# Optimization experiments

Hardware: AMD Instinct MI355X
Metric: run time of the kernel (lower is better)

The kernel has to match this reference:

```python
import jax, jax.numpy as jnp
import numpy as np
from jax import lax

B, L, H, O, T = 256, 2, 256, 256, 512


def setup_inputs() -> dict:
    key = jax.random.key(0)
    ks = jax.random.split(key, 9)
    s = 0.1  # keep gates out of saturation
    return {
        "x": jax.random.normal(ks[0], (B, 1, H), jnp.float32),
        "h0": jax.random.normal(ks[1], (L, B, H), jnp.float32) * s,
        "c0": jax.random.normal(ks[2], (L, B, H), jnp.float32) * s,
        "W_ih": jax.random.normal(ks[3], (L, 4 * H, H), jnp.float32) * s,
        "W_hh": jax.random.normal(ks[4], (L, 4 * H, H), jnp.float32) * s,
        "b_ih": jax.random.normal(ks[5], (L, 4 * H), jnp.float32) * s,
        "b_hh": jax.random.normal(ks[6], (L, 4 * H), jnp.float32) * s,
        "fc_w": jax.random.normal(ks[7], (O, H), jnp.float32) * s,
        "fc_b": jax.random.normal(ks[8], (O,), jnp.float32) * s,
        "max_length": T,
    }


def _lstm_cell(inp, h, c, Wi, Wh, bi, bh):
    # PyTorch gate order: i, f, g, o
    gates = inp @ Wi.T + h @ Wh.T + bi + bh  # [B, 4H]
    i, f, g, o = jnp.split(gates, 4, axis=-1)
    i = jax.nn.sigmoid(i)
    f = jax.nn.sigmoid(f)
    g = jnp.tanh(g)
    o = jax.nn.sigmoid(o)
    c_new = f * c + i * g
    h_new = o * jnp.tanh(c_new)
    return h_new, c_new


def reference(x, h0, c0, W_ih, W_hh, b_ih, b_hh, fc_w, fc_b, max_length):
    n_layers = W_ih.shape[0]
    xin = x[:, 0, :]  # same single-step input re-fed every iteration

    def step(carry, _):
        h, c = carry  # each [L, B, H]
        inp = xin
        hs, cs = [], []
        for l in range(n_layers):
            hl, cl = _lstm_cell(inp, h[l], c[l], W_ih[l], W_hh[l], b_ih[l], b_hh[l])
            hs.append(hl)
            cs.append(cl)
            inp = hl
        return (jnp.stack(hs), jnp.stack(cs)), inp  # last-layer hidden

    _, outs = lax.scan(step, (h0, c0), None, length=max_length)  # [T, B, H]
    seq = jnp.transpose(outs, (1, 0, 2))  # [B, T, H]
    logits = seq @ fc_w.T + fc_b  # [B, T, O]
    return jax.nn.log_softmax(logits, axis=-1), jax.nn.softmax(logits, axis=-1)
```

## Files before the change

### kernel.cpp

```cpp
#include <hip/hip_runtime.h>

#define TSTEPS 512
#define BATCH  256
#define HID    256
#define OUTC   256

typedef _Float16 half8 __attribute__((ext_vector_type(8)));
typedef float    f32x4 __attribute__((ext_vector_type(4)));

union G16 { unsigned long long u2[2]; unsigned u[4]; half8 h; };

#define H0_SLOTS 16
#define H1_SLOTS 4
#define H0RING_QW (H0_SLOTS*16*16*128)
#define H1RING_QW (H1_SLOTS*16*16*128)
#define FLAG_DW   (16*TSTEPS)

__device__ __forceinline__ float sigf(float x){ return 1.0f/(1.0f+__expf(-x)); }
__device__ __forceinline__ float tanh_(float x){
  float a = fminf(fmaxf(x,-8.0f),8.0f);
  float e = __expf(2.0f*a);
  return (e-1.0f)/(e+1.0f);
}
__device__ __forceinline__ void st64(unsigned long long* p, unsigned long long v){
  __hip_atomic_store(p, v, __ATOMIC_RELAXED, __HIP_MEMORY_SCOPE_AGENT);
}
__device__ __forceinline__ unsigned long long ld64(const unsigned long long* p){
  return __hip_atomic_load(p, __ATOMIC_RELAXED, __HIP_MEMORY_SCOPE_AGENT);
}
__device__ __forceinline__ unsigned pack2(float a, float b){
  _Float16 x=(_Float16)a, y=(_Float16)b;
  return (unsigned)__builtin_bit_cast(unsigned short,x)
       | ((unsigned)__builtin_bit_cast(unsigned short,y)<<16);
}

__global__ void prep_convert(const float* __restrict__ Wih, const float* __restrict__ Whh,
                             const float* __restrict__ fcw, const float* __restrict__ bih,
                             const float* __restrict__ bhh,
                             _Float16* __restrict__ wh0, _Float16* __restrict__ wi1,
                             _Float16* __restrict__ wh1, _Float16* __restrict__ fcwh,
                             float* __restrict__ bias1)
{
  int i = blockIdx.x*256 + threadIdx.x;
  wh0[i] = (_Float16)Whh[i];
  wi1[i] = (_Float16)Wih[262144 + i];
  wh1[i] = (_Float16)Whh[262144 + i];
  if (i < 65536) fcwh[i] = (_Float16)fcw[i];
  if (i < 1024)  bias1[i] = bih[1024+i] + bhh[1024+i];
}

__global__ void prep_gx0(const float* __restrict__ x, const float* __restrict__ Wih,
                         const float* __restrict__ bih, const float* __restrict__ bhh,
                         float* __restrict__ gx0)
{
  int gid = blockIdx.x*256 + threadIdx.x;
  int b = gid >> 10, n = gid & 1023;
  const float4* xv = (const float4*)(x + (size_t)b*256);
  const float4* wv = (const float4*)(Wih + (size_t)n*256);
  float s = bih[n] + bhh[n];
  #pragma unroll 8
  for (int k=0;k<64;k++){
    float4 a = xv[k], c = wv[k];
    s += a.x*c.x + a.y*c.y + a.z*c.z + a.w*c.w;
  }
  gx0[gid] = s;
}

__global__ void zero_scratch(unsigned long long* __restrict__ base){
  size_t i = (size_t)blockIdx.x*256 + threadIdx.x;
  st64(base + i, 0ull);
}

__global__ void seed_rings(const float* __restrict__ h_in,
                           unsigned long long* __restrict__ h0ring,
                           unsigned long long* __restrict__ h1ring)
{
  int idx = blockIdx.x*256 + threadIdx.x;
  int b = idx >> 7, pair = idx & 127;
  int grp = b >> 4, row = b & 15;
  const float* s0 = h_in + (size_t)b*256 + 2*pair;
  const float* s1 = s0 + 65536;
  unsigned long long v0 = (1ull<<32) | pack2(s0[0], s0[1]);
  unsigned long long v1 = (1ull<<32) | pack2(s1[0], s1[1]);
  st64(&h0ring[(((size_t)15*16+grp)*16+row)*128 + pair], v0);
  st64(&h1ring[(((size_t) 3*16+grp)*16+row)*128 + pair], v1);
}

__device__ __forceinline__ void poll_tile(const unsigned long long* __restrict__ ring,
                                          int slot, int grp, unsigned tag,
                                          _Float16* __restrict__ shdst, int tid)
{
  int row = tid >> 5, q = tid & 31;
  const unsigned long long* p = ring + (((size_t)slot*16+grp)*16 + row)*128 + q*4;
  unsigned long long v0,v1,v2,v3;
  for (;;){
    v0 = ld64(p);   v1 = ld64(p+1);
    v2 = ld64(p+2); v3 = ld64(p+3);
    if ((unsigned)(v0>>32)==tag && (unsigned)(v1>>32)==tag &&
        (unsigned)(v2>>32)==tag && (unsigned)(v3>>32)==tag) break;
    __builtin_amdgcn_s_sleep(1);
  }
  G16 g;
  g.u[0]=(unsigned)v0; g.u[1]=(unsigned)v1; g.u[2]=(unsigned)v2; g.u[3]=(unsigned)v3;
  *(half8*)&shdst[row*256 + (q ^ (row&7))*8] = g.h;
}

__global__ __launch_bounds__(512,1) void lstm_fused(
    const float* __restrict__ gx0, const _Float16* __restrict__ Wh0g,
    const _Float16* __restrict__ Wi1g, const _Float16* __restrict__ Wh1g,
    const float* __restrict__ bias1, const float* __restrict__ c0_in,
    unsigned* __restrict__ seq1dw,
    unsigned long long* __restrict__ h0ring,
    unsigned long long* __restrict__ h1ring,
    unsigned* __restrict__ flagC)
{
  __shared__ __align__(16) _Float16 Ws[65536];
  __shared__ __align__(16) _Float16 shA[4096];
  __shared__ __align__(16) char     Rg[16896];
  const int blk = blockIdx.x;
  const int tid = threadIdx.x;
  const int wv  = tid >> 6, l = tid & 63;
  const int c16 = l & 15, kg = l >> 4;

  if (blk < 64){
    const int grp = blk >> 2, s = blk & 3;
    const int b0  = grp*16;
    const int gate = wv >> 1, jblk = (wv & 1)*32;
    float (*gbuf)[16][66] = (float (*)[16][66])Rg;

    for (int idx = tid; idx < 8192; idx += 512){
      int row = idx >> 5, gr = idx & 31;
      int g = row >> 6, jl = row & 63;
      half8 v = *(const half8*)(Wh0g + ((size_t)(g*256 + s*64 + jl))*256 + gr*8);
      *(half8*)&Ws[row*256 + (gr ^ (row&7))*8] = v;
    }
    const int eb = tid >> 5, jp = tid & 31;
    float cA = c0_in[(size_t)(b0+eb)*256 + s*64 + 2*jp];
    float cB = c0_in[(size_t)(b0+eb)*256 + s*64 + 2*jp + 1];
    float gxr[2][4];
    #pragma unroll
    for (int nt=0;nt<2;nt++)
      #pragma unroll
      for (int r=0;r<4;r++)
        gxr[nt][r] = gx0[(size_t)(b0 + kg*4 + r)*1024 + gate*256 + s*64 + jblk + nt*16 + c16];
    const int r0 = gate*64 + jblk + c16;
    const int r1 = r0 + 16;
    __syncthreads();

    for (int t = 0; t < TSTEPS; ++t){
      poll_tile(h0ring, (t-1)&(H0_SLOTS-1), grp, (unsigned)(t+1), shA, tid);
      if (tid == 0 && t >= H0_SLOTS){
        const unsigned* f = flagC + grp*TSTEPS + (t - H0_SLOTS);
        while (__hip_atomic_load(f, __ATOMIC_RELAXED, __HIP_MEMORY_SCOPE_AGENT) < 8u)
          __builtin_amdgcn_s_sleep(2);
      }
      __syncthreads();

      f32x4 acc0 = { gxr[0][0], gxr[0][1], gxr[0][2], gxr[0][3] };
      f32x4 acc1 = { gxr[1][0], gxr[1][1], gxr[1][2], gxr[1][3] };
      #pragma unroll
      for (int kt=0;kt<8;kt++){
        half8 af  = *(const half8*)&shA[c16*256 + ((kt*4+kg) ^ (c16&7))*8];
        half8 b0f = *(const half8*)&Ws[r0*256 + ((kt*4+kg) ^ (r0&7))*8];
        half8 b1f = *(const half8*)&Ws[r1*256 + ((kt*4+kg) ^ (r1&7))*8];
        acc0 = __builtin_amdgcn_mfma_f32_16x16x32_f16(af, b0f, acc0, 0,0,0);
        acc1 = __builtin_amdgcn_mfma_f32_16x16x32_f16(af, b1f, acc1, 0,0,0);
      }
      #pragma unroll
      for (int r=0;r<4;r++){
        gbuf[gate][kg*4+r][jblk + c16]      = acc0[r];
        gbuf[gate][kg*4+r][jblk + 16 + c16] = acc1[r];
      }
      __syncthreads();
      {
        int j0 = 2*jp, j1 = 2*jp+1;
        float i0 = sigf (gbuf[0][eb][j0]), i1 = sigf (gbuf[0][eb][j1]);
        float f0 = sigf (gbuf[1][eb][j0]), f1 = sigf (gbuf[1][eb][j1]);
        float g0 = tanh_(gbuf[2][eb][j0]), g1 = tanh_(gbuf[2][eb][j1]);
        float o0 = sigf (gbuf[3][eb][j0]), o1 = sigf (gbuf[3][eb][j1]);
        cA = f0*cA + i0*g0;
        cB = f1*cB + i1*g1;
        unsigned d = pack2(o0*tanh_(cA), o1*tanh_(cB));
        st64(&h0ring[(((size_t)(t&(H0_SLOTS-1))*16+grp)*16+eb)*128 + s*32+jp],
             ((unsigned long long)(unsigned)(t+2)<<32) | d);
      }
    }
  } else {
    const int bb  = blk - 64;
    const int grp = bb >> 3, js = bb & 7;
    const int b0  = grp*16, jb = js*32;
    const int gate = wv >> 1, jhalf = (wv & 1)*16;
    _Float16* sh1 = (_Float16*)Rg;
    float (*gbuf)[16][34] = (float (*)[16][34])(Rg + 8192);

    for (int idx = tid; idx < 8192; idx += 512){
      int row = idx >> 6, gr = idx & 63;
      int g = row >> 5, jl = row & 31;
      size_t nrow = (size_t)(g*256 + jb + jl);
      const _Float16* src = (gr < 32) ? (Wi1g + nrow*256 + gr*8)
                                      : (Wh1g + nrow*256 + (size_t)(gr-32)*8);
      *(half8*)&Ws[row*512 + (gr ^ (row&7))*8] = *(const half8*)src;
    }
    const int eb = tid >> 4, jp = tid & 15;
    float cA = 0.f, cB = 0.f;
    if (tid < 256){
      cA = c0_in[65536 + (size_t)(b0+eb)*256 + jb + 2*jp];
      cB = c0_in[65536 + (size_t)(b0+eb)*256 + jb + 2*jp + 1];
    }
    const float bv = bias1[gate*256 + jb + jhalf + c16];
    const int nl = gate*32 + jhalf + c16;
    __syncthreads();

    for (int t = 0; t < TSTEPS; ++t){
      poll_tile(h0ring, t&(H0_SLOTS-1), grp, (unsigned)(t+2), shA, tid);
      __syncthreads();
      if (tid == 0)
        __hip_atomic_fetch_add(flagC + grp*TSTEPS + t, 1u,
                               __ATOMIC_RELAXED, __HIP_MEMORY_SCOPE_AGENT);
      f32x4 acc = { bv, bv, bv, bv };
      #pragma unroll
      for (int kt=0;kt<8;kt++){
        half8 af = *(const half8*)&shA[c16*256 + ((kt*4+kg) ^ (c16&7))*8];
        half8 bf = *(const half8*)&Ws[nl*512 + ((kt*4+kg) ^ (nl&7))*8];
        acc = __builtin_amdgcn_mfma_f32_16x16x32_f16(af, bf, acc, 0,0,0);
      }
      poll_tile(h1ring, (t-1)&(H1_SLOTS-1), grp, (unsigned)(t+1), sh1, tid);
      __syncthreads();
      #pragma unroll
      for (int kt=0;kt<8;kt++){
        half8 af = *(const half8*)&sh1[c16*256 + ((kt*4+kg) ^ (c16&7))*8];
        half8 bf = *(const half8*)&Ws[nl*512 + ((32 + kt*4+kg) ^ (nl&7))*8];
        acc = __builtin_amdgcn_mfma_f32_16x16x32_f16(af, bf, acc, 0,0,0);
      }
      #pragma unroll
      for (int r=0;r<4;r++) gbuf[gate][kg*4+r][jhalf + c16] = acc[r];
      __syncthreads();
      if (tid < 256){
        int j0 = 2*jp, j1 = 2*jp+1;
        float i0 = sigf (gbuf[0][eb][j0]), i1 = sigf (gbuf[0][eb][j1]);
        float f0 = sigf (gbuf[1][eb][j0]), f1 = sigf (gbuf[1][eb][j1]);
        float g0 = tanh_(gbuf[2][eb][j0]), g1 = tanh_(gbuf[2][eb][j1]);
        float o0 = sigf (gbuf[3][eb][j0]), o1 = sigf (gbuf[3][eb][j1]);
        cA = f0*cA + i0*g0;
        cB = f1*cB + i1*g1;
        unsigned d = pack2(o0*tanh_(cA), o1*tanh_(cB));
        st64(&h1ring[(((size_t)(t&(H1_SLOTS-1))*16+grp)*16+eb)*128 + js*16+jp],
             ((unsigned long long)(unsigned)(t+2)<<32) | d);
        seq1dw[((size_t)(b0+eb)*TSTEPS + t)*256 + js*16 + jp] = d;
      }
    }
  }
}

__global__ __launch_bounds__(256) void fc_kernel(
    const _Float16* __restrict__ seq, int pitch,
    const _Float16* __restrict__ fcwh, const float* __restrict__ fcb,
    float* __restrict__ out0, float* __restrict__ out1)
{
  const int tid = threadIdx.x;
  const int w = tid >> 6, l = tid & 63;
  const int col = l & 15, kg = l >> 4;
  const size_t m0 = (size_t)blockIdx.x*64 + (size_t)w*16;
  half8 a[8];
  #pragma unroll
  for (int kt=0;kt<8;kt++)
    a[kt] = *(const half8*)&seq[(m0+col)*(size_t)pitch + kt*32 + kg*8];
  f32x4 acc[16];
  #pragma unroll
  for (int nt=0;nt<16;nt++){
    int n = nt*16 + col;
    float bvl = fcb[n];
    f32x4 c = {bvl,bvl,bvl,bvl};
    const _Float16* wr = fcwh + (size_t)n*256;
    #pragma unroll
    for (int kt=0;kt<8;kt++){
      half8 bf = *(const half8*)&wr[kt*32 + kg*8];
      c = __builtin_amdgcn_mfma_f32_16x16x32_f16(a[kt], bf, c, 0,0,0);
    }
    acc[nt] = c;
  }
  #pragma unroll
  for (int r=0;r<4;r++){
    float mx = -3.0e38f;
    #pragma unroll
    for (int nt=0;nt<16;nt++) mx = fmaxf(mx, acc[nt][r]);
    #pragma unroll
    for (int off=1; off<16; off<<=1) mx = fmaxf(mx, __shfl_xor(mx, off, 64));
    float s = 0.0f;
    #pragma unroll
    for (int nt=0;nt<16;nt++) s += __expf(acc[nt][r]-mx);
    #pragma unroll
    for (int off=1; off<16; off<<=1) s += __shfl_xor(s, off, 64);
    float inv = 1.0f/s;
    float ls  = __logf(s);
    size_t row = m0 + (size_t)kg*4 + r;
    #pragma unroll
    for (int nt=0;nt<16;nt++){
      int n = nt*16 + col;
      float v = acc[nt][r]-mx;
      out0[row*256 + n] = v - ls;
      out1[row*256 + n] = __expf(v)*inv;
    }
  }
}

extern "C" void kernel_launch(void* const* d_in, const int* in_sizes, int n_in,
                              void* d_out, int out_size, void* d_ws, size_t ws_size,
                              hipStream_t stream)
{
  const float* x   = (const float*)d_in[0];
  const float* h0  = (const float*)d_in[1];
  const float* c0  = (const float*)d_in[2];
  const float* Wih = (const float*)d_in[3];
  const float* Whh = (const float*)d_in[4];
  const float* bih = (const float*)d_in[5];
  const float* bhh = (const float*)d_in[6];
  const float* fcw = (const float*)d_in[7];
  const float* fcb = (const float*)d_in[8];
  (void)in_sizes; (void)n_in; (void)out_size; (void)ws_size;

  char* ws = (char*)d_ws;
  _Float16* wh0   = (_Float16*)(ws + 0);
  _Float16* wi1   = (_Float16*)(ws + (512<<10));
  _Float16* wh1   = (_Float16*)(ws + (1024<<10));
  _Float16* fcwh  = (_Float16*)(ws + (1536<<10));
  float*    bias1 = (float*)   (ws + (1664<<10));
  float*    gx0   = (float*)   (ws + (1668<<10));

  float* out0 = (float*)d_out;
  float* out1 = out0 + (size_t)BATCH*TSTEPS*OUTC;
  unsigned long long* h0ring = (unsigned long long*)d_out;
  unsigned long long* h1ring = h0ring + H0RING_QW;
  unsigned*           flagC  = (unsigned*)(h1ring + H1RING_QW);
  unsigned* seq1dw = (unsigned*)out1;
  _Float16* seq1   = (_Float16*)out1;

  const int zeroQW = H0RING_QW + H1RING_QW + FLAG_DW/2;
  hipLaunchKernelGGL(zero_scratch, dim3(zeroQW/256), dim3(256), 0, stream, h0ring);
  hipLaunchKernelGGL(prep_convert, dim3(1024), dim3(256), 0, stream,
                     Wih, Whh, fcw, bih, bhh, wh0, wi1, wh1, fcwh, bias1);
  hipLaunchKernelGGL(prep_gx0, dim3(1024), dim3(256), 0, stream,
                     x, Wih, bih, bhh, gx0);
  hipLaunchKernelGGL(seed_rings, dim3(128), dim3(256), 0, stream, h0, h0ring, h1ring);
  hipLaunchKernelGGL(lstm_fused, dim3(192), dim3(512), 0, stream,
                     gx0, wh0, wi1, wh1, bias1, c0, seq1dw, h0ring, h1ring, flagC);
  hipLaunchKernelGGL(fc_kernel, dim3(2048), dim3(256), 0, stream,
                     seq1, 512, fcwh, fcb, out0, out1);
}
```

Before: 1.835 ms.

## Rework LSTM inter-block sync: local h reuse, batched flags, prefetch polls

Blocks now write their own freshly computed h slice straight into shared memory and only poll the ring for the slices other blocks produced. The initial hidden state is loaded directly from the inputs, so the seed_rings kernel is gone. The per-step flagC counter with atomic fetch_add is replaced by a per-block progress word that is stored every 8 steps and checked every 8 steps, which shrinks the flag area that must be zeroed. Layer-1 blocks prefetch the next h0 tile before they need it. Polling drops s_sleep and uses wave-wide __all checks. All of this aims to cut cross-block synchronisation latency on the serial recurrence, at the cost of spinning harder and a subtler ring-reuse margin (h0 slots vs the 8-step flag granularity).

```diff
diff --git a/kernel.cpp b/kernel.cpp
--- a/kernel.cpp
+++ b/kernel.cpp
@@ -7,14 +7,12 @@
 
 typedef _Float16 half8 __attribute__((ext_vector_type(8)));
 typedef float    f32x4 __attribute__((ext_vector_type(4)));
-
 union G16 { unsigned long long u2[2]; unsigned u[4]; half8 h; };
 
 #define H0_SLOTS 16
 #define H1_SLOTS 4
 #define H0RING_QW (H0_SLOTS*16*16*128)
 #define H1RING_QW (H1_SLOTS*16*16*128)
-#define FLAG_DW   (16*TSTEPS)
 
 __device__ __forceinline__ float sigf(float x){ return 1.0f/(1.0f+__expf(-x)); }
 __device__ __forceinline__ float tanh_(float x){
@@ -26,6 +24,12 @@
   __hip_atomic_store(p, v, __ATOMIC_RELAXED, __HIP_MEMORY_SCOPE_AGENT);
 }
 __device__ __forceinline__ unsigned long long ld64(const unsigned long long* p){
+  return __hip_atomic_load(p, __ATOMIC_RELAXED, __HIP_MEMORY_SCOPE_AGENT);
+}
+__device__ __forceinline__ void st32(unsigned* p, unsigned v){
+  __hip_atomic_store(p, v, __ATOMIC_RELAXED, __HIP_MEMORY_SCOPE_AGENT);
+}
+__device__ __forceinline__ unsigned ld32(const unsigned* p){
   return __hip_atomic_load(p, __ATOMIC_RELAXED, __HIP_MEMORY_SCOPE_AGENT);
 }
 __device__ __forceinline__ unsigned pack2(float a, float b){
@@ -66,103 +70,72 @@
   gx0[gid] = s;
 }
 
-__global__ void zero_scratch(unsigned long long* __restrict__ base){
-  size_t i = (size_t)blockIdx.x*256 + threadIdx.x;
-  st64(base + i, 0ull);
-}
-
-__global__ void seed_rings(const float* __restrict__ h_in,
-                           unsigned long long* __restrict__ h0ring,
-                           unsigned long long* __restrict__ h1ring)
-{
-  int idx = blockIdx.x*256 + threadIdx.x;
-  int b = idx >> 7, pair = idx & 127;
-  int grp = b >> 4, row = b & 15;
-  const float* s0 = h_in + (size_t)b*256 + 2*pair;
-  const float* s1 = s0 + 65536;
-  unsigned long long v0 = (1ull<<32) | pack2(s0[0], s0[1]);
-  unsigned long long v1 = (1ull<<32) | pack2(s1[0], s1[1]);
-  st64(&h0ring[(((size_t)15*16+grp)*16+row)*128 + pair], v0);
-  st64(&h1ring[(((size_t) 3*16+grp)*16+row)*128 + pair], v1);
-}
-
-__device__ __forceinline__ void poll_tile(const unsigned long long* __restrict__ ring,
-                                          int slot, int grp, unsigned tag,
-                                          _Float16* __restrict__ shdst, int tid)
-{
-  int row = tid >> 5, q = tid & 31;
-  const unsigned long long* p = ring + (((size_t)slot*16+grp)*16 + row)*128 + q*4;
-  unsigned long long v0,v1,v2,v3;
-  for (;;){
-    v0 = ld64(p);   v1 = ld64(p+1);
-    v2 = ld64(p+2); v3 = ld64(p+3);
-    if ((unsigned)(v0>>32)==tag && (unsigned)(v1>>32)==tag &&
-        (unsigned)(v2>>32)==tag && (unsigned)(v3>>32)==tag) break;
-    __builtin_amdgcn_s_sleep(1);
-  }
-  G16 g;
-  g.u[0]=(unsigned)v0; g.u[1]=(unsigned)v1; g.u[2]=(unsigned)v2; g.u[3]=(unsigned)v3;
-  *(half8*)&shdst[row*256 + (q ^ (row&7))*8] = g.h;
-}
-
-__global__ __launch_bounds__(512,1) void lstm_fused(
+__global__ void zero_scratch(unsigned long long* __restrict__ base, int total){
+  int i = blockIdx.x*256 + threadIdx.x;
+  if (i < total) st64(base + i, 0ull);
+}
+
+__global__ __launch_bounds__(512,1) void lstm4(
     const float* __restrict__ gx0, const _Float16* __restrict__ Wh0g,
     const _Float16* __restrict__ Wi1g, const _Float16* __restrict__ Wh1g,
-    const float* __restrict__ bias1, const float* __restrict__ c0_in,
-    unsigned* __restrict__ seq1dw,
-    unsigned long long* __restrict__ h0ring,
-    unsigned long long* __restrict__ h1ring,
+    const float* __restrict__ bias1, const float* __restrict__ h_in,
+    const float* __restrict__ c_in, unsigned* __restrict__ seq1dw,
+    unsigned long long* __restrict__ h0r, unsigned long long* __restrict__ h1r,
     unsigned* __restrict__ flagC)
 {
-  __shared__ __align__(16) _Float16 Ws[65536];
-  __shared__ __align__(16) _Float16 shA[4096];
-  __shared__ __align__(16) char     Rg[16896];
-  const int blk = blockIdx.x;
-  const int tid = threadIdx.x;
-  const int wv  = tid >> 6, l = tid & 63;
-  const int c16 = l & 15, kg = l >> 4;
+  __shared__ __align__(16) char Lb[156160];
+  _Float16* Ws  = (_Float16*)Lb;
+  _Float16* sh0 = (_Float16*)(Lb + 131072);
+
+  const int blk = blockIdx.x, tid = threadIdx.x;
+  const int wv = tid>>6, l = tid&63, c16 = l&15, kg = l>>4;
 
   if (blk < 64){
-    const int grp = blk >> 2, s = blk & 3;
-    const int b0  = grp*16;
-    const int gate = wv >> 1, jblk = (wv & 1)*32;
-    float (*gbuf)[16][66] = (float (*)[16][66])Rg;
-
-    for (int idx = tid; idx < 8192; idx += 512){
-      int row = idx >> 5, gr = idx & 31;
-      int g = row >> 6, jl = row & 63;
+    const int grp = blk>>2, s = blk&3, b0 = grp*16;
+    const int gate = wv>>1, jblk = (wv&1)*32;
+    float (*gbuf)[16][66] = (float (*)[16][66])(Lb + 139264);
+
+    for (int idx=tid; idx<8192; idx+=512){
+      int row = idx>>5, gr = idx&31;
+      int g = row>>6, jl = row&63;
       half8 v = *(const half8*)(Wh0g + ((size_t)(g*256 + s*64 + jl))*256 + gr*8);
-      *(half8*)&Ws[row*256 + (gr ^ (row&7))*8] = v;
-    }
-    const int eb = tid >> 5, jp = tid & 31;
-    float cA = c0_in[(size_t)(b0+eb)*256 + s*64 + 2*jp];
-    float cB = c0_in[(size_t)(b0+eb)*256 + s*64 + 2*jp + 1];
+      *(half8*)&Ws[row*256 + (gr^(row&7))*8] = v;
+    }
+    { int row = tid>>5, q = tid&31;
+      const float* sp = h_in + (size_t)(b0+row)*256 + q*8;
+      half8 v;
+      #pragma unroll
+      for (int qq=0;qq<8;qq++) v[qq] = (_Float16)sp[qq];
+      *(half8*)&sh0[row*256 + (q^(row&7))*8] = v; }
+    const int eb = tid>>5, jp = tid&31;
+    float cA = c_in[(size_t)(b0+eb)*256 + s*64 + 2*jp];
+    float cB = c_in[(size_t)(b0+eb)*256 + s*64 + 2*jp + 1];
     float gxr[2][4];
     #pragma unroll
     for (int nt=0;nt<2;nt++)
       #pragma unroll
       for (int r=0;r<4;r++)
         gxr[nt][r] = gx0[(size_t)(b0 + kg*4 + r)*1024 + gate*256 + s*64 + jblk + nt*16 + c16];
-    const int r0 = gate*64 + jblk + c16;
-    const int r1 = r0 + 16;
+    const int r0 = gate*64 + jblk + c16, r1 = r0 + 16;
     __syncthreads();
 
-    for (int t = 0; t < TSTEPS; ++t){
-      poll_tile(h0ring, (t-1)&(H0_SLOTS-1), grp, (unsigned)(t+1), shA, tid);
-      if (tid == 0 && t >= H0_SLOTS){
-        const unsigned* f = flagC + grp*TSTEPS + (t - H0_SLOTS);
-        while (__hip_atomic_load(f, __ATOMIC_RELAXED, __HIP_MEMORY_SCOPE_AGENT) < 8u)
-          __builtin_amdgcn_s_sleep(2);
-      }
-      __syncthreads();
-
+    for (int t=0; t<TSTEPS; ++t){
+      if (((t&7)==0) && t>=16 && tid<64){
+        const unsigned need = (unsigned)(t-8);
+        bool ok;
+        do {
+          unsigned v = need;
+          if (tid < 8) v = ld32(&flagC[grp*8 + tid]);
+          ok = (v >= need);
+        } while (!__all(ok));
+      }
       f32x4 acc0 = { gxr[0][0], gxr[0][1], gxr[0][2], gxr[0][3] };
       f32x4 acc1 = { gxr[1][0], gxr[1][1], gxr[1][2], gxr[1][3] };
       #pragma unroll
       for (int kt=0;kt<8;kt++){
-        half8 af  = *(const half8*)&shA[c16*256 + ((kt*4+kg) ^ (c16&7))*8];
-        half8 b0f = *(const half8*)&Ws[r0*256 + ((kt*4+kg) ^ (r0&7))*8];
-        half8 b1f = *(const half8*)&Ws[r1*256 + ((kt*4+kg) ^ (r1&7))*8];
+        half8 af  = *(const half8*)&sh0[c16*256 + ((kt*4+kg)^(c16&7))*8];
+        half8 b0f = *(const half8*)&Ws[r0*256 + ((kt*4+kg)^(r0&7))*8];
+        half8 b1f = *(const half8*)&Ws[r1*256 + ((kt*4+kg)^(r1&7))*8];
         acc0 = __builtin_amdgcn_mfma_f32_16x16x32_f16(af, b0f, acc0, 0,0,0);
         acc1 = __builtin_amdgcn_mfma_f32_16x16x32_f16(af, b1f, acc1, 0,0,0);
       }
@@ -180,56 +153,113 @@
         float o0 = sigf (gbuf[3][eb][j0]), o1 = sigf (gbuf[3][eb][j1]);
         cA = f0*cA + i0*g0;
         cB = f1*cB + i1*g1;
-        unsigned d = pack2(o0*tanh_(cA), o1*tanh_(cB));
-        st64(&h0ring[(((size_t)(t&(H0_SLOTS-1))*16+grp)*16+eb)*128 + s*32+jp],
-             ((unsigned long long)(unsigned)(t+2)<<32) | d);
-      }
+        unsigned pk = pack2(o0*tanh_(cA), o1*tanh_(cB));
+        int jg = s*64 + j0;
+        *(unsigned*)&sh0[eb*256 + ((jg>>3)^(eb&7))*8 + (jg&7)] = pk;
+        st64(&h0r[(((size_t)(t&(H0_SLOTS-1))*16+grp)*16 + eb)*128 + s*32 + jp],
+             (((unsigned long long)(unsigned)(t+2))<<32) | pk);
+      }
+      {
+        int row = tid>>5, q = tid&31;
+        if ((q>>3) != s){
+          const unsigned long long* p =
+            h0r + (((size_t)(t&(H0_SLOTS-1))*16+grp)*16 + row)*128 + q*4;
+          unsigned tg32 = (unsigned)(t+2);
+          unsigned long long v0,v1,v2,v3;
+          for(;;){
+            v0=ld64(p); v1=ld64(p+1); v2=ld64(p+2); v3=ld64(p+3);
+            bool ok = (unsigned)(v0>>32)==tg32 && (unsigned)(v1>>32)==tg32 &&
+                      (unsigned)(v2>>32)==tg32 && (unsigned)(v3>>32)==tg32;
+            if (__all(ok)) break;
+          }
+          G16 g; g.u[0]=(unsigned)v0; g.u[1]=(unsigned)v1;
+                 g.u[2]=(unsigned)v2; g.u[3]=(unsigned)v3;
+          *(half8*)&sh0[row*256 + (q^(row&7))*8] = g.h;
+        }
+      }
+      __syncthreads();
     }
   } else {
-    const int bb  = blk - 64;
-    const int grp = bb >> 3, js = bb & 7;
-    const int b0  = grp*16, jb = js*32;
-    const int gate = wv >> 1, jhalf = (wv & 1)*16;
-    _Float16* sh1 = (_Float16*)Rg;
-    float (*gbuf)[16][34] = (float (*)[16][34])(Rg + 8192);
-
-    for (int idx = tid; idx < 8192; idx += 512){
-      int row = idx >> 6, gr = idx & 63;
-      int g = row >> 5, jl = row & 31;
+    const int bb = blk-64, grp = bb>>3, js = bb&7;
+    const int b0 = grp*16, jb = js*32;
+    const int gate = wv>>1, jhalf = (wv&1)*16;
+    _Float16* sh1 = (_Float16*)(Lb + 139264);
+    float (*gbuf)[16][34] = (float (*)[16][34])(Lb + 147456);
+
+    for (int idx=tid; idx<8192; idx+=512){
+      int row = idx>>6, gr = idx&63;
+      int g = row>>5, jl = row&31;
       size_t nrow = (size_t)(g*256 + jb + jl);
       const _Float16* src = (gr < 32) ? (Wi1g + nrow*256 + gr*8)
                                       : (Wh1g + nrow*256 + (size_t)(gr-32)*8);
-      *(half8*)&Ws[row*512 + (gr ^ (row&7))*8] = *(const half8*)src;
-    }
-    const int eb = tid >> 4, jp = tid & 15;
+      *(half8*)&Ws[row*512 + (gr^(row&7))*8] = *(const half8*)src;
+    }
+    { int row = tid>>5, q = tid&31;
+      const float* sp = h_in + 65536 + (size_t)(b0+row)*256 + q*8;
+      half8 v;
+      #pragma unroll
+      for (int qq=0;qq<8;qq++) v[qq] = (_Float16)sp[qq];
+      *(half8*)&sh1[row*256 + (q^(row&7))*8] = v; }
+    const int eb = tid>>4, jp = tid&15;
     float cA = 0.f, cB = 0.f;
     if (tid < 256){
-      cA = c0_in[65536 + (size_t)(b0+eb)*256 + jb + 2*jp];
-      cB = c0_in[65536 + (size_t)(b0+eb)*256 + jb + 2*jp + 1];
+      cA = c_in[65536 + (size_t)(b0+eb)*256 + jb + 2*jp];
+      cB = c_in[65536 + (size_t)(b0+eb)*256 + jb + 2*jp + 1];
     }
     const float bv = bias1[gate*256 + jb + jhalf + c16];
     const int nl = gate*32 + jhalf + c16;
+    const int prow = tid>>5, pq = tid&31;
+    unsigned long long hv0,hv1,hv2,hv3;
+    {
+      const unsigned long long* p = h0r + (((size_t)grp)*16 + prow)*128 + pq*4;
+      hv0=ld64(p); hv1=ld64(p+1); hv2=ld64(p+2); hv3=ld64(p+3);
+    }
     __syncthreads();
 
-    for (int t = 0; t < TSTEPS; ++t){
-      poll_tile(h0ring, t&(H0_SLOTS-1), grp, (unsigned)(t+2), shA, tid);
-      __syncthreads();
-      if (tid == 0)
-        __hip_atomic_fetch_add(flagC + grp*TSTEPS + t, 1u,
-                               __ATOMIC_RELAXED, __HIP_MEMORY_SCOPE_AGENT);
+    for (int t=0; t<TSTEPS; ++t){
+      {
+        unsigned tg32 = (unsigned)(t+2);
+        const unsigned long long* p =
+          h0r + (((size_t)(t&(H0_SLOTS-1))*16+grp)*16 + prow)*128 + pq*4;
+        for(;;){
+          bool ok = (unsigned)(hv0>>32)==tg32 && (unsigned)(hv1>>32)==tg32 &&
+                    (unsigned)(hv2>>32)==tg32 && (unsigned)(hv3>>32)==tg32;
+          if (__all(ok)) break;
+          hv0=ld64(p); hv1=ld64(p+1); hv2=ld64(p+2); hv3=ld64(p+3);
+        }
+        G16 g; g.u[0]=(unsigned)hv0; g.u[1]=(unsigned)hv1;
+               g.u[2]=(unsigned)hv2; g.u[3]=(unsigned)hv3;
+        *(half8*)&sh0[prow*256 + (pq^(prow&7))*8] = g.h;
+      }
+      __syncthreads();
+      if (((t&7)==0) && tid==0) st32(&flagC[grp*8+js], (unsigned)t);
       f32x4 acc = { bv, bv, bv, bv };
       #pragma unroll
       for (int kt=0;kt<8;kt++){
-        half8 af = *(const half8*)&shA[c16*256 + ((kt*4+kg) ^ (c16&7))*8];
-        half8 bf = *(const half8*)&Ws[nl*512 + ((kt*4+kg) ^ (nl&7))*8];
+        half8 af = *(const half8*)&sh0[c16*256 + ((kt*4+kg)^(c16&7))*8];
+        half8 bf = *(const half8*)&Ws[nl*512 + ((kt*4+kg)^(nl&7))*8];
         acc = __builtin_amdgcn_mfma_f32_16x16x32_f16(af, bf, acc, 0,0,0);
       }
-      poll_tile(h1ring, (t-1)&(H1_SLOTS-1), grp, (unsigned)(t+1), sh1, tid);
+      if (t > 0 && (pq>>2) != js){
+        const unsigned long long* p =
+          h1r + (((size_t)((t+3)&(H1_SLOTS-1))*16+grp)*16 + prow)*128 + pq*4;
+        unsigned tg32 = (unsigned)(t+1);
+        unsigned long long v0,v1,v2,v3;
+        for(;;){
+          v0=ld64(p); v1=ld64(p+1); v2=ld64(p+2); v3=ld64(p+3);
+          bool ok = (unsigned)(v0>>32)==tg32 && (unsigned)(v1>>32)==tg32 &&
+                    (unsigned)(v2>>32)==tg32 && (unsigned)(v3>>32)==tg32;
+          if (__all(ok)) break;
+        }
+        G16 g; g.u[0]=(unsigned)v0; g.u[1]=(unsigned)v1;
+               g.u[2]=(unsigned)v2; g.u[3]=(unsigned)v3;
+        *(half8*)&sh1[prow*256 + (pq^(prow&7))*8] = g.h;
+      }
       __syncthreads();
       #pragma unroll
       for (int kt=0;kt<8;kt++){
-        half8 af = *(const half8*)&sh1[c16*256 + ((kt*4+kg) ^ (c16&7))*8];
-        half8 bf = *(const half8*)&Ws[nl*512 + ((32 + kt*4+kg) ^ (nl&7))*8];
+        half8 af = *(const half8*)&sh1[c16*256 + ((kt*4+kg)^(c16&7))*8];
+        half8 bf = *(const half8*)&Ws[nl*512 + ((32+kt*4+kg)^(nl&7))*8];
         acc = __builtin_amdgcn_mfma_f32_16x16x32_f16(af, bf, acc, 0,0,0);
       }
       #pragma unroll
@@ -243,10 +273,17 @@
         float o0 = sigf (gbuf[3][eb][j0]), o1 = sigf (gbuf[3][eb][j1]);
         cA = f0*cA + i0*g0;
         cB = f1*cB + i1*g1;
-        unsigned d = pack2(o0*tanh_(cA), o1*tanh_(cB));
-        st64(&h1ring[(((size_t)(t&(H1_SLOTS-1))*16+grp)*16+eb)*128 + js*16+jp],
-             ((unsigned long long)(unsigned)(t+2)<<32) | d);
-        seq1dw[((size_t)(b0+eb)*TSTEPS + t)*256 + js*16 + jp] = d;
+        unsigned pk = pack2(o0*tanh_(cA), o1*tanh_(cB));
+        int jg = jb + j0;
+        *(unsigned*)&sh1[eb*256 + ((jg>>3)^(eb&7))*8 + (jg&7)] = pk;
+        st64(&h1r[(((size_t)(t&(H1_SLOTS-1))*16+grp)*16 + eb)*128 + js*16 + jp],
+             (((unsigned long long)(unsigned)(t+2))<<32) | pk);
+        seq1dw[((size_t)(b0+eb)*TSTEPS + t)*256 + js*16 + jp] = pk;
+      }
+      if (t+1 < TSTEPS){
+        const unsigned long long* p =
+          h0r + (((size_t)((t+1)&(H0_SLOTS-1))*16+grp)*16 + prow)*128 + pq*4;
+        hv0=ld64(p); hv1=ld64(p+1); hv2=ld64(p+2); hv3=ld64(p+3);
       }
     }
   }
@@ -327,23 +364,25 @@
   float*    bias1 = (float*)   (ws + (1664<<10));
   float*    gx0   = (float*)   (ws + (1668<<10));
 
+  char* ob = (char*)d_out;
   float* out0 = (float*)d_out;
   float* out1 = out0 + (size_t)BATCH*TSTEPS*OUTC;
-  unsigned long long* h0ring = (unsigned long long*)d_out;
-  unsigned long long* h1ring = h0ring + H0RING_QW;
-  unsigned*           flagC  = (unsigned*)(h1ring + H1RING_QW);
+  unsigned long long* h0r   = (unsigned long long*)ob;
+  unsigned long long* h1r   = h0r + H0RING_QW;
+  unsigned*           flagC = (unsigned*)(h1r + H1RING_QW);
   unsigned* seq1dw = (unsigned*)out1;
   _Float16* seq1   = (_Float16*)out1;
 
-  const int zeroQW = H0RING_QW + H1RING_QW + FLAG_DW/2;
-  hipLaunchKernelGGL(zero_scratch, dim3(zeroQW/256), dim3(256), 0, stream, h0ring);
+  const int zeroQW = H0RING_QW + H1RING_QW + 64;
+  hipLaunchKernelGGL(zero_scratch, dim3((zeroQW+255)/256), dim3(256), 0, stream,
+                     h0r, zeroQW);
   hipLaunchKernelGGL(prep_convert, dim3(1024), dim3(256), 0, stream,
                      Wih, Whh, fcw, bih, bhh, wh0, wi1, wh1, fcwh, bias1);
   hipLaunchKernelGGL(prep_gx0, dim3(1024), dim3(256), 0, stream,
                      x, Wih, bih, bhh, gx0);
-  hipLaunchKernelGGL(seed_rings, dim3(128), dim3(256), 0, stream, h0, h0ring, h1ring);
-  hipLaunchKernelGGL(lstm_fused, dim3(192), dim3(512), 0, stream,
-                     gx0, wh0, wi1, wh1, bias1, c0, seq1dw, h0ring, h1ring, flagC);
+  hipLaunchKernelGGL(lstm4, dim3(192), dim3(512), 0, stream,
+                     gx0, wh0, wi1, wh1, bias1, h0, c0,
+                     seq1dw, h0r, h1r, flagC);
   hipLaunchKernelGGL(fc_kernel, dim3(2048), dim3(256), 0, stream,
                      seq1, 512, fcwh, fcb, out0, out1);
 }
```

After: 1.810 ms. No clear change (-1.3%).
